# Performance work log

Measured on AMD Instinct MI355X. Metric: run time of the kernel, lower is better.

The kernel has to match this reference:

```python
import jax, jax.numpy as jnp
import numpy as np

ALPHA, GAMMA, EPS = 0.25, 2.0, 1e-8
COST_CLASS, COST_BBOX, COST_GIOU = 2.0, 5.0, 2.0


def box_cxcywh_to_xyxy(b):
    cx, cy, w, h = jnp.split(b, 4, axis=-1)
    return jnp.concatenate([cx - 0.5 * w, cy - 0.5 * h, cx + 0.5 * w, cy + 0.5 * h], axis=-1)


def setup_inputs() -> dict:
    key = jax.random.key(0)
    k1, k2, k3, k4 = jax.random.split(key, 4)
    bs, Q, C, T = 16, 900, 80, 1600
    return {
        "pred_logits": jax.random.normal(k1, (bs, Q, C), jnp.float32),
        "pred_boxes": jax.random.uniform(k2, (bs, Q, 4), jnp.float32),
        "tgt_labels": jax.random.randint(k3, (T,), 0, C),
        "tgt_boxes": jax.random.uniform(k4, (T, 4), jnp.float32),
        "g_size": 3,
    }


def reference(pred_logits, pred_boxes, tgt_labels, tgt_boxes, g_size):
    bs, Q, _ = pred_logits.shape
    # focal classification cost (use_focal=True path)
    p = jax.nn.sigmoid(pred_logits.reshape(bs * Q, -1))  # [N, C]
    neg = (1.0 - ALPHA) * p ** GAMMA * (-jnp.log(1.0 - p + EPS))
    pos = ALPHA * (1.0 - p) ** GAMMA * (-jnp.log(p + EPS))
    cost_class = (pos - neg)[:, tgt_labels]  # [N, T]
    # L1 box cost (cdist p=1)
    out_bbox = pred_boxes.reshape(bs * Q, 4)
    cost_bbox = jnp.abs(out_bbox[:, None, :] - tgt_bbox_b(tgt_boxes)).sum(-1)  # [N, T]
    # GIoU cost
    b1 = box_cxcywh_to_xyxy(out_bbox)  # [N, 4]
    b2 = box_cxcywh_to_xyxy(tgt_boxes)  # [T, 4]
    area1 = (b1[:, 2] - b1[:, 0]) * (b1[:, 3] - b1[:, 1])
    area2 = (b2[:, 2] - b2[:, 0]) * (b2[:, 3] - b2[:, 1])
    lt = jnp.maximum(b1[:, None, :2], b2[None, :, :2])
    rb = jnp.minimum(b1[:, None, 2:], b2[None, :, 2:])
    wh = jnp.clip(rb - lt, 0.0)
    inter = wh[..., 0] * wh[..., 1]
    union = area1[:, None] + area2[None, :] - inter
    iou = inter / union
    elt = jnp.minimum(b1[:, None, :2], b2[None, :, :2])
    erb = jnp.maximum(b1[:, None, 2:], b2[None, :, 2:])
    ewh = jnp.clip(erb - elt, 0.0)
    earea = ewh[..., 0] * ewh[..., 1]
    giou = iou - (earea - union) / earea
    # weighted total cost, then group reduction (note: original names it Cmin but takes max over the group dim)
    Cmat = COST_BBOX * cost_bbox + COST_CLASS * cost_class + COST_GIOU * (-giou)
    Cmin = Cmat.reshape(bs, Q // g_size, g_size, -1).max(axis=2)  # [bs, Q//g, T]
    return Cmin


def tgt_bbox_b(tgt_boxes):
    return tgt_boxes[None, :, :]
```

## Files before the change

kernel.cpp:

```cpp
#include <hip/hip_runtime.h>

#define ALPHA 0.25f
#define EPS   1e-8f

constexpr int BS = 16;
constexpr int QN = 900;
constexpr int CN = 80;
constexpr int GS = 3;
constexpr int QG_PER_BLOCK = 4;
constexpr int ROWS = QG_PER_BLOCK * GS;
constexpr int NT_THREADS = 256;
constexpr int TSPLIT = 2;

__global__ __launch_bounds__(NT_THREADS) void fused_cost_kernel(
    const float* __restrict__ pred_logits,
    const float* __restrict__ pred_boxes,
    const int*   __restrict__ tgt_labels,
    const float* __restrict__ tgt_boxes,
    float*       __restrict__ out,
    int T)
{
    __shared__ __align__(16) float s_cc_t[CN * ROWS];

    const int tid = threadIdx.x;
    const int qg0 = blockIdx.y * QG_PER_BLOCK;
    const int b   = blockIdx.z;
    const int n0  = b * QN + qg0 * GS;

    const float* lg0 = pred_logits + (size_t)n0 * CN;
    for (int k = tid; k < ROWS * CN; k += NT_THREADS) {
        const int r = k / CN, c = k - r * CN;
        float x = lg0[k];
        float p = __fdividef(1.0f, 1.0f + __expf(-x));
        float omp = 1.0f - p;
        float pos = ALPHA * omp * omp * (-__logf(p + EPS));
        float neg = (1.0f - ALPHA) * p * p * (-__logf(omp + EPS));
        s_cc_t[c * ROWS + r] = pos - neg;
    }

    float Pcx[ROWS], Pcy[ROWS], Pw[ROWS], Ph[ROWS];
    float Px0[ROWS], Py0[ROWS], Px1[ROWS], Py1[ROWS];
    #pragma unroll
    for (int r = 0; r < ROWS; ++r) {
        const float4 pb = ((const float4*)pred_boxes)[n0 + r];
        Pcx[r] = pb.x;  Pcy[r] = pb.y;  Pw[r] = pb.z;  Ph[r] = pb.w;
        Px0[r] = pb.x - 0.5f * pb.z;  Py0[r] = pb.y - 0.5f * pb.w;
        Px1[r] = pb.x + 0.5f * pb.z;  Py1[r] = pb.y + 0.5f * pb.w;
    }
    __syncthreads();

    const int tChunk = T / TSPLIT;
    const int t0 = blockIdx.x * tChunk;
    const int tEnd = t0 + tChunk;
    const int qgTotal = QN / GS;
    const size_t outBase = (size_t)(b * qgTotal + qg0) * T;

    for (int t = t0 + tid; t < tEnd; t += NT_THREADS) {
        const float4 tr = ((const float4*)tgt_boxes)[t];
        const int lab   = tgt_labels[t];
        const float tx0 = tr.x - 0.5f * tr.z, ty0 = tr.y - 0.5f * tr.w;
        const float tx1 = tr.x + 0.5f * tr.z, ty1 = tr.y + 0.5f * tr.w;
        const float ta  = tr.z * tr.w;

        const float4* ccp = (const float4*)&s_cc_t[lab * ROWS];
        const float4 c0 = ccp[0], c1 = ccp[1], c2 = ccp[2];
        const float ccv[ROWS] = { c0.x, c0.y, c0.z, c0.w,
                                  c1.x, c1.y, c1.z, c1.w,
                                  c2.x, c2.y, c2.z, c2.w };

        #pragma unroll
        for (int j = 0; j < QG_PER_BLOCK; ++j) {
            float m = -3.402823466e+38f;
            #pragma unroll
            for (int g = 0; g < GS; ++g) {
                const int idx = j * GS + g;

                float l1 = fabsf(Pcx[idx] - tr.x) + fabsf(Pcy[idx] - tr.y)
                         + fabsf(Pw[idx]  - tr.z) + fabsf(Ph[idx]  - tr.w);

                float iw = fminf(Px1[idx], tx1) - fmaxf(Px0[idx], tx0);
                float ih = fminf(Py1[idx], ty1) - fmaxf(Py0[idx], ty0);
                float inter = fmaxf(iw, 0.0f) * fmaxf(ih, 0.0f);
                float uni   = Pw[idx] * Ph[idx] + ta - inter;

                float ew = fmaxf(Px1[idx], tx1) - fminf(Px0[idx], tx0);
                float eh = fmaxf(Py1[idx], ty1) - fminf(Py0[idx], ty0);
                float earea = ew * eh;

                float num = fmaf(inter, earea, uni * uni);
                float den = uni * earea;
                float g2  = 2.0f * __fdividef(num, den);

                float cost = fmaf(5.0f, l1, fmaf(2.0f, ccv[idx], 2.0f - g2));
                m = fmaxf(m, cost);
            }
            out[outBase + (size_t)j * T + t] = m;
        }
    }
}

extern "C" void kernel_launch(void* const* d_in, const int* in_sizes, int n_in,
                              void* d_out, int out_size, void* d_ws, size_t ws_size,
                              hipStream_t stream) {
    const float* pred_logits = (const float*)d_in[0];
    const float* pred_boxes  = (const float*)d_in[1];
    const int*   tgt_labels  = (const int*)d_in[2];
    const float* tgt_boxes   = (const float*)d_in[3];

    const int T = in_sizes[2];
    float* out = (float*)d_out;

    dim3 grid(TSPLIT, (QN / GS) / QG_PER_BLOCK, BS);
    fused_cost_kernel<<<grid, NT_THREADS, 0, stream>>>(
        pred_logits, pred_boxes, tgt_labels, tgt_boxes, out, T);
}
```

Measured before the change: 102.4 us.

## Assign one query group per wave and loop waves over all targets

Result: slower. 104.9 us (+2.5%).

```diff
diff --git a/kernel.cpp b/kernel.cpp
--- a/kernel.cpp
+++ b/kernel.cpp
@@ -3,16 +3,16 @@
 #define ALPHA 0.25f
 #define EPS   1e-8f
 
-constexpr int BS = 16;
-constexpr int QN = 900;
-constexpr int CN = 80;
-constexpr int GS = 3;
-constexpr int QG_PER_BLOCK = 4;
-constexpr int ROWS = QG_PER_BLOCK * GS;
-constexpr int NT_THREADS = 256;
-constexpr int TSPLIT = 2;
+constexpr int BS    = 16;
+constexpr int QN    = 900;
+constexpr int CN    = 80;
+constexpr int GS    = 3;
+constexpr int WAVES = 4;
+constexpr int NT    = WAVES * 64;
+constexpr int ROWS  = WAVES * GS;
+constexpr int CCPAD = 16;
 
-__global__ __launch_bounds__(NT_THREADS) void fused_cost_kernel(
+__global__ __launch_bounds__(NT) void fused_cost_kernel(
     const float* __restrict__ pred_logits,
     const float* __restrict__ pred_boxes,
     const int*   __restrict__ tgt_labels,
@@ -20,82 +20,74 @@
     float*       __restrict__ out,
     int T)
 {
-    __shared__ __align__(16) float s_cc_t[CN * ROWS];
+    __shared__ __align__(16) float s_cc[CN * CCPAD];
 
-    const int tid = threadIdx.x;
-    const int qg0 = blockIdx.y * QG_PER_BLOCK;
-    const int b   = blockIdx.z;
-    const int n0  = b * QN + qg0 * GS;
+    const int tid  = threadIdx.x;
+    const int wv   = tid >> 6;
+    const int lane = tid & 63;
+    const int b    = blockIdx.y;
+    const int n0   = b * QN + blockIdx.x * ROWS;
 
     const float* lg0 = pred_logits + (size_t)n0 * CN;
-    for (int k = tid; k < ROWS * CN; k += NT_THREADS) {
+    for (int k = tid; k < ROWS * CN; k += NT) {
         const int r = k / CN, c = k - r * CN;
         float x = lg0[k];
         float p = __fdividef(1.0f, 1.0f + __expf(-x));
         float omp = 1.0f - p;
         float pos = ALPHA * omp * omp * (-__logf(p + EPS));
         float neg = (1.0f - ALPHA) * p * p * (-__logf(omp + EPS));
-        s_cc_t[c * ROWS + r] = pos - neg;
+        s_cc[c * CCPAD + r + r / GS] = pos - neg;
     }
 
-    float Pcx[ROWS], Pcy[ROWS], Pw[ROWS], Ph[ROWS];
-    float Px0[ROWS], Py0[ROWS], Px1[ROWS], Py1[ROWS];
+    float Pcx[GS], Pcy[GS], Pw[GS], Ph[GS];
+    float Px0[GS], Py0[GS], Px1[GS], Py1[GS], Pa[GS];
     #pragma unroll
-    for (int r = 0; r < ROWS; ++r) {
-        const float4 pb = ((const float4*)pred_boxes)[n0 + r];
-        Pcx[r] = pb.x;  Pcy[r] = pb.y;  Pw[r] = pb.z;  Ph[r] = pb.w;
-        Px0[r] = pb.x - 0.5f * pb.z;  Py0[r] = pb.y - 0.5f * pb.w;
-        Px1[r] = pb.x + 0.5f * pb.z;  Py1[r] = pb.y + 0.5f * pb.w;
+    for (int g = 0; g < GS; ++g) {
+        const float4 pb = ((const float4*)pred_boxes)[n0 + wv * GS + g];
+        Pcx[g] = pb.x;  Pcy[g] = pb.y;  Pw[g] = pb.z;  Ph[g] = pb.w;
+        Px0[g] = pb.x - 0.5f * pb.z;  Py0[g] = pb.y - 0.5f * pb.w;
+        Px1[g] = pb.x + 0.5f * pb.z;  Py1[g] = pb.y + 0.5f * pb.w;
+        Pa[g]  = pb.z * pb.w;
     }
     __syncthreads();
 
-    const int tChunk = T / TSPLIT;
-    const int t0 = blockIdx.x * tChunk;
-    const int tEnd = t0 + tChunk;
-    const int qgTotal = QN / GS;
-    const size_t outBase = (size_t)(b * qgTotal + qg0) * T;
+    const int qg = blockIdx.x * WAVES + wv;
+    float* __restrict__ outp = out + (size_t)(b * (QN / GS) + qg) * T;
+    const int ccBase = wv * 4;
 
-    for (int t = t0 + tid; t < tEnd; t += NT_THREADS) {
+    for (int t = lane; t < T; t += 64) {
         const float4 tr = ((const float4*)tgt_boxes)[t];
         const int lab   = tgt_labels[t];
         const float tx0 = tr.x - 0.5f * tr.z, ty0 = tr.y - 0.5f * tr.w;
         const float tx1 = tr.x + 0.5f * tr.z, ty1 = tr.y + 0.5f * tr.w;
         const float ta  = tr.z * tr.w;
 
-        const float4* ccp = (const float4*)&s_cc_t[lab * ROWS];
-        const float4 c0 = ccp[0], c1 = ccp[1], c2 = ccp[2];
-        const float ccv[ROWS] = { c0.x, c0.y, c0.z, c0.w,
-                                  c1.x, c1.y, c1.z, c1.w,
-                                  c2.x, c2.y, c2.z, c2.w };
+        const float4 cc4 = *(const float4*)&s_cc[lab * CCPAD + ccBase];
+        const float ccv[GS] = { cc4.x, cc4.y, cc4.z };
 
+        float m = -3.402823466e+38f;
         #pragma unroll
-        for (int j = 0; j < QG_PER_BLOCK; ++j) {
-            float m = -3.402823466e+38f;
-            #pragma unroll
-            for (int g = 0; g < GS; ++g) {
-                const int idx = j * GS + g;
+        for (int g = 0; g < GS; ++g) {
+            float l1 = fabsf(Pcx[g] - tr.x) + fabsf(Pcy[g] - tr.y)
+                     + fabsf(Pw[g]  - tr.z) + fabsf(Ph[g]  - tr.w);
 
-                float l1 = fabsf(Pcx[idx] - tr.x) + fabsf(Pcy[idx] - tr.y)
-                         + fabsf(Pw[idx]  - tr.z) + fabsf(Ph[idx]  - tr.w);
+            float iw = fminf(Px1[g], tx1) - fmaxf(Px0[g], tx0);
+            float ih = fminf(Py1[g], ty1) - fmaxf(Py0[g], ty0);
+            float inter = fmaxf(iw, 0.0f) * fmaxf(ih, 0.0f);
+            float uni   = Pa[g] + ta - inter;
 
-                float iw = fminf(Px1[idx], tx1) - fmaxf(Px0[idx], tx0);
-                float ih = fminf(Py1[idx], ty1) - fmaxf(Py0[idx], ty0);
-                float inter = fmaxf(iw, 0.0f) * fmaxf(ih, 0.0f);
-                float uni   = Pw[idx] * Ph[idx] + ta - inter;
+            float ew = fmaxf(Px1[g], tx1) - fminf(Px0[g], tx0);
+            float eh = fmaxf(Py1[g], ty1) - fminf(Py0[g], ty0);
+            float earea = ew * eh;
 
-                float ew = fmaxf(Px1[idx], tx1) - fminf(Px0[idx], tx0);
-                float eh = fmaxf(Py1[idx], ty1) - fminf(Py0[idx], ty0);
-                float earea = ew * eh;
+            float num = fmaf(inter, earea, uni * uni);
+            float den = uni * earea;
+            float g2  = 2.0f * __fdividef(num, den);
 
-                float num = fmaf(inter, earea, uni * uni);
-                float den = uni * earea;
-                float g2  = 2.0f * __fdividef(num, den);
-
-                float cost = fmaf(5.0f, l1, fmaf(2.0f, ccv[idx], 2.0f - g2));
-                m = fmaxf(m, cost);
-            }
-            out[outBase + (size_t)j * T + t] = m;
+            float cost = fmaf(5.0f, l1, fmaf(2.0f, ccv[g], 2.0f - g2));
+            m = fmaxf(m, cost);
         }
+        outp[t] = m;
     }
 }
 
@@ -110,7 +102,7 @@
     const int T = in_sizes[2];
     float* out = (float*)d_out;
 
-    dim3 grid(TSPLIT, (QN / GS) / QG_PER_BLOCK, BS);
-    fused_cost_kernel<<<grid, NT_THREADS, 0, stream>>>(
+    dim3 grid((QN / GS) / WAVES, BS);
+    fused_cost_kernel<<<grid, NT, 0, stream>>>(
         pred_logits, pred_boxes, tgt_labels, tgt_boxes, out, T);
 }
```
